# Optimization experiments

Hardware: AMD Instinct MI355X
Metric: run time of the kernel (lower is better)

The kernel has to match this reference:

```python
import jax, jax.numpy as jnp
import numpy as np

EPS = 1e-12  # torch F.normalize default eps

def _l1_normalize(x):
    # F.normalize(x, p=1, dim=1): divide by channel-wise L1 norm, clamped at eps
    n = jnp.sum(jnp.abs(x), axis=1, keepdims=True)
    return x / jnp.maximum(n, EPS)

def setup_inputs() -> dict:
    key = jax.random.key(0)
    k1, k2, k3 = jax.random.split(key, 3)
    shape = (2, 128, 64, 64)  # B, C, H, W
    return {
        "a": jax.random.normal(k1, shape, dtype=jnp.float32),
        "b": jax.random.normal(k2, shape, dtype=jnp.float32),
        "c": jax.random.normal(k3, shape, dtype=jnp.float32),
    }

def reference(a, b, c):
    a = _l1_normalize(a)
    b = _l1_normalize(b)
    c = _l1_normalize(c)
    sim_ab = jnp.einsum('bchw,bcij->bhwij', a, b)
    sim_ac = jnp.einsum('bchw,bcij->bhwij', a, c)
    # F.l1_loss default reduction='mean'
    return jnp.mean(jnp.abs(sim_ac - sim_ab))
```

## Files before the change

kernel.cpp:

```cpp
#include <hip/hip_runtime.h>
#include <stdint.h>

#define HW 4096
#define NC 128
#define BATCH 2

typedef __attribute__((ext_vector_type(8))) short bf16x8;
typedef __attribute__((ext_vector_type(4))) float f32x4;
typedef __attribute__((ext_vector_type(8))) unsigned short u16x8;

__device__ __forceinline__ unsigned short f32_to_bf16(float f) {
    union { float f; unsigned int u; } v; v.f = f;
    unsigned int u = v.u;
    unsigned int r = (u + 0x7FFFu + ((u >> 16) & 1u)) >> 16;
    return (unsigned short)r;
}

__device__ __forceinline__ void async_cp16(const void* g, void* s) {
    __builtin_amdgcn_global_load_lds(
        (const __attribute__((address_space(1))) uint32_t*)g,
        (__attribute__((address_space(3))) uint32_t*)s, 16, 0, 0);
}

__global__ __launch_bounds__(512) void norm_kernel(
    const float* __restrict__ A, const float* __restrict__ B,
    const float* __restrict__ Cc,
    unsigned short* __restrict__ anT, unsigned short* __restrict__ dT,
    float* __restrict__ out) {
    const int tid = threadIdx.x;
    if (blockIdx.x == 0 && tid == 0) *out = 0.f;
    const int pl = tid & 31;
    const int cg = tid >> 5;
    const int gp = blockIdx.x * 32;
    const int bb = gp >> 12;
    const int p  = (gp & (HW - 1)) + pl;
    const size_t base = (size_t)bb * NC * HW + p;
    const int c0 = cg * 8;

    float va[8], vb[8], vc[8];
    float sa = 0.f, sb = 0.f, sc = 0.f;
#pragma unroll
    for (int k = 0; k < 8; ++k) {
        size_t idx = base + (size_t)(c0 + k) * HW;
        va[k] = A[idx]; vb[k] = B[idx]; vc[k] = Cc[idx];
        sa += fabsf(va[k]); sb += fabsf(vb[k]); sc += fabsf(vc[k]);
    }
    __shared__ float red[3][16][32];
    red[0][cg][pl] = sa; red[1][cg][pl] = sb; red[2][cg][pl] = sc;
    __syncthreads();
    float na = 0.f, nb = 0.f, nc = 0.f;
#pragma unroll
    for (int g = 0; g < 16; ++g) {
        na += red[0][g][pl]; nb += red[1][g][pl]; nc += red[2][g][pl];
    }
    const float ra = 1.f / fmaxf(na, 1e-12f);
    const float rb = 1.f / fmaxf(nb, 1e-12f);
    const float rc = 1.f / fmaxf(nc, 1e-12f);

    const size_t obase = ((size_t)bb * HW + p) * NC;
    const int slot = cg ^ (p & 15);
    u16x8 xa, xd;
#pragma unroll
    for (int j = 0; j < 8; ++j) {
        xa[j] = f32_to_bf16(va[j] * ra);
        xd[j] = f32_to_bf16(vc[j] * rc - vb[j] * rb);
    }
    *(u16x8*)(anT + obase + slot * 8) = xa;
    *(u16x8*)(dT  + obase + slot * 8) = xd;
}

__global__ __launch_bounds__(256, 2) void simloss_kernel(
    const unsigned short* __restrict__ anT, const unsigned short* __restrict__ dT,
    float* __restrict__ out) {
    __shared__ uint4 smem4[4096];
    const int tid = threadIdx.x;
    const int b   = blockIdx.x;
    const int bz  = b >> 8;
    const int my  = (b & 255) >> 3;
    const int ng  = b & 7;
    const char* gA = (const char*)(anT + ((size_t)bz * HW + my * 128) * NC);
    const char* gB0 = (const char*)(dT + ((size_t)bz * HW + ng * 4 * 128) * NC);

    const int wv  = tid >> 6;
    const int ln  = tid & 63;
    char* sA = (char*)smem4;
    char* sB = (char*)(smem4 + 2048);

#pragma unroll
    for (int i = 0; i < 8; ++i) {
        const size_t goff = (size_t)(i * 256 + tid) * 16;
        const size_t loff = (size_t)i * 4096 + wv * 1024;
        async_cp16(gA + goff, sA + loff);
        async_cp16(gB0 + goff, sB + loff);
    }
    __syncthreads();

    const int m16  = ln & 15;
    const int quad = ln >> 4;
    const int wr   = (wv >> 1) * 64;
    const int wc   = (wv & 1) * 64;

    float s = 0.f;
    for (int j = 0; j < 4; ++j) {
        f32x4 acc[4][4] = {};
#pragma unroll
        for (int ks = 0; ks < 4; ++ks) {
            const int chunk = ks * 4 + quad;
            const int slot  = chunk ^ m16;
            bf16x8 af[4], bfr[4];
#pragma unroll
            for (int mi = 0; mi < 4; ++mi)
                af[mi] = *(const bf16x8*)(sA + (wr + mi * 16 + m16) * 256 + slot * 16);
#pragma unroll
            for (int ni = 0; ni < 4; ++ni)
                bfr[ni] = *(const bf16x8*)(sB + (wc + ni * 16 + m16) * 256 + slot * 16);
#pragma unroll
            for (int mi = 0; mi < 4; ++mi)
#pragma unroll
                for (int ni = 0; ni < 4; ++ni)
                    acc[mi][ni] = __builtin_amdgcn_mfma_f32_16x16x32_bf16(
                        af[mi], bfr[ni], acc[mi][ni], 0, 0, 0);
        }
#pragma unroll
        for (int mi = 0; mi < 4; ++mi)
#pragma unroll
            for (int ni = 0; ni < 4; ++ni)
#pragma unroll
                for (int r = 0; r < 4; ++r)
                    s += fabsf(acc[mi][ni][r]);

        __syncthreads();
        if (j < 3) {
            const char* gBn = gB0 + (size_t)(j + 1) * 32768;
#pragma unroll
            for (int i = 0; i < 8; ++i) {
                const size_t goff = (size_t)(i * 256 + tid) * 16;
                const size_t loff = (size_t)i * 4096 + wv * 1024;
                async_cp16(gBn + goff, sB + loff);
            }
            __syncthreads();
        }
    }

#pragma unroll
    for (int off = 32; off > 0; off >>= 1)
        s += __shfl_down(s, off);
    if (ln == 0) ((float*)smem4)[wv] = s;
    __syncthreads();
    if (tid == 0) {
        const float inv = 1.0f / ((float)BATCH * (float)HW * (float)HW);
        float t = ((float*)smem4)[0] + ((float*)smem4)[1] +
                  ((float*)smem4)[2] + ((float*)smem4)[3];
        atomicAdd(out, t * inv);
    }
}

extern "C" void kernel_launch(void* const* d_in, const int* in_sizes, int n_in,
                              void* d_out, int out_size, void* d_ws, size_t ws_size,
                              hipStream_t stream) {
    const float* A  = (const float*)d_in[0];
    const float* B  = (const float*)d_in[1];
    const float* Cc = (const float*)d_in[2];
    float* out = (float*)d_out;
    unsigned short* anT = (unsigned short*)d_ws;
    unsigned short* dT  = anT + (size_t)BATCH * HW * NC;

    norm_kernel<<<dim3(256), dim3(512), 0, stream>>>(A, B, Cc, anT, dT, out);
    simloss_kernel<<<dim3(512), dim3(256), 0, stream>>>(anT, dT, out);
}
```

Baseline: 79.71 us.

## Fuse normalize and similarity-loss kernels with a grid barrier; register-prefetch B tiles

Merges the normalization pass and the MFMA similarity-loss pass into one persistent launch of 512 blocks, separated by a software grid-wide barrier built on a global atomic counter. This removes a kernel launch and the gap between the two kernels. It also replaces the async global-to-LDS copies of the next B tile with register prefetches issued before the MFMA loop and written to LDS afterward, so the loads overlap compute. The risks are deadlock if all 512 blocks are not co-resident, barrier spin overhead, and higher register pressure from the prefetch buffers.

```diff
diff --git a/kernel.cpp b/kernel.cpp
--- a/kernel.cpp
+++ b/kernel.cpp
@@ -4,10 +4,13 @@
 #define HW 4096
 #define NC 128
 #define BATCH 2
+#define NBLK 512
 
 typedef __attribute__((ext_vector_type(8))) short bf16x8;
 typedef __attribute__((ext_vector_type(4))) float f32x4;
 typedef __attribute__((ext_vector_type(8))) unsigned short u16x8;
+
+__device__ unsigned int g_barrier = 0;
 
 __device__ __forceinline__ unsigned short f32_to_bf16(float f) {
     union { float f; unsigned int u; } v; v.f = f;
@@ -22,67 +25,81 @@
         (__attribute__((address_space(3))) uint32_t*)s, 16, 0, 0);
 }
 
-__global__ __launch_bounds__(512) void norm_kernel(
+__global__ __launch_bounds__(256, 2) void fused_kernel(
     const float* __restrict__ A, const float* __restrict__ B,
     const float* __restrict__ Cc,
     unsigned short* __restrict__ anT, unsigned short* __restrict__ dT,
     float* __restrict__ out) {
-    const int tid = threadIdx.x;
-    if (blockIdx.x == 0 && tid == 0) *out = 0.f;
-    const int pl = tid & 31;
-    const int cg = tid >> 5;
-    const int gp = blockIdx.x * 32;
-    const int bb = gp >> 12;
-    const int p  = (gp & (HW - 1)) + pl;
-    const size_t base = (size_t)bb * NC * HW + p;
-    const int c0 = cg * 8;
-
-    float va[8], vb[8], vc[8];
-    float sa = 0.f, sb = 0.f, sc = 0.f;
-#pragma unroll
-    for (int k = 0; k < 8; ++k) {
-        size_t idx = base + (size_t)(c0 + k) * HW;
-        va[k] = A[idx]; vb[k] = B[idx]; vc[k] = Cc[idx];
-        sa += fabsf(va[k]); sb += fabsf(vb[k]); sc += fabsf(vc[k]);
-    }
-    __shared__ float red[3][16][32];
-    red[0][cg][pl] = sa; red[1][cg][pl] = sb; red[2][cg][pl] = sc;
-    __syncthreads();
-    float na = 0.f, nb = 0.f, nc = 0.f;
-#pragma unroll
-    for (int g = 0; g < 16; ++g) {
-        na += red[0][g][pl]; nb += red[1][g][pl]; nc += red[2][g][pl];
-    }
-    const float ra = 1.f / fmaxf(na, 1e-12f);
-    const float rb = 1.f / fmaxf(nb, 1e-12f);
-    const float rc = 1.f / fmaxf(nc, 1e-12f);
-
-    const size_t obase = ((size_t)bb * HW + p) * NC;
-    const int slot = cg ^ (p & 15);
-    u16x8 xa, xd;
-#pragma unroll
-    for (int j = 0; j < 8; ++j) {
-        xa[j] = f32_to_bf16(va[j] * ra);
-        xd[j] = f32_to_bf16(vc[j] * rc - vb[j] * rb);
-    }
-    *(u16x8*)(anT + obase + slot * 8) = xa;
-    *(u16x8*)(dT  + obase + slot * 8) = xd;
-}
-
-__global__ __launch_bounds__(256, 2) void simloss_kernel(
-    const unsigned short* __restrict__ anT, const unsigned short* __restrict__ dT,
-    float* __restrict__ out) {
     __shared__ uint4 smem4[4096];
     const int tid = threadIdx.x;
     const int b   = blockIdx.x;
+
+    {
+        if (b == 0 && tid == 0) *out = 0.f;
+        const int pl = tid & 15;
+        const int cg = tid >> 4;
+        const int gp = b * 16;
+        const int bb = gp >> 12;
+        const int p  = (gp & (HW - 1)) + pl;
+        const size_t base = (size_t)bb * NC * HW + p;
+        const int c0 = cg * 8;
+
+        float va[8], vb[8], vc[8];
+        float sa = 0.f, sb = 0.f, sc = 0.f;
+#pragma unroll
+        for (int k = 0; k < 8; ++k) {
+            size_t idx = base + (size_t)(c0 + k) * HW;
+            va[k] = A[idx]; vb[k] = B[idx]; vc[k] = Cc[idx];
+            sa += fabsf(va[k]); sb += fabsf(vb[k]); sc += fabsf(vc[k]);
+        }
+        float* red = (float*)smem4;
+        red[(0 * 16 + cg) * 16 + pl] = sa;
+        red[(1 * 16 + cg) * 16 + pl] = sb;
+        red[(2 * 16 + cg) * 16 + pl] = sc;
+        __syncthreads();
+        float na = 0.f, nb = 0.f, nc = 0.f;
+#pragma unroll
+        for (int g = 0; g < 16; ++g) {
+            na += red[(0 * 16 + g) * 16 + pl];
+            nb += red[(1 * 16 + g) * 16 + pl];
+            nc += red[(2 * 16 + g) * 16 + pl];
+        }
+        const float ra = 1.f / fmaxf(na, 1e-12f);
+        const float rb = 1.f / fmaxf(nb, 1e-12f);
+        const float rc = 1.f / fmaxf(nc, 1e-12f);
+
+        const size_t obase = ((size_t)bb * HW + p) * NC;
+        const int slot = cg ^ (p & 15);
+        u16x8 xa, xd;
+#pragma unroll
+        for (int j = 0; j < 8; ++j) {
+            xa[j] = f32_to_bf16(va[j] * ra);
+            xd[j] = f32_to_bf16(vc[j] * rc - vb[j] * rb);
+        }
+        *(u16x8*)(anT + obase + slot * 8) = xa;
+        *(u16x8*)(dT  + obase + slot * 8) = xd;
+    }
+
+    __threadfence();
+    __syncthreads();
+    if (tid == 0) {
+        unsigned int old = atomicAdd(&g_barrier, 1u);
+        unsigned int target = (old & ~(unsigned)(NBLK - 1)) + NBLK;
+        while ((int)(__hip_atomic_load(&g_barrier, __ATOMIC_RELAXED,
+                                       __HIP_MEMORY_SCOPE_AGENT) - target) < 0)
+            __builtin_amdgcn_s_sleep(2);
+    }
+    __syncthreads();
+    __threadfence();
+
     const int bz  = b >> 8;
     const int my  = (b & 255) >> 3;
     const int ng  = b & 7;
-    const char* gA = (const char*)(anT + ((size_t)bz * HW + my * 128) * NC);
-    const char* gB0 = (const char*)(dT + ((size_t)bz * HW + ng * 4 * 128) * NC);
+    const char* gA  = (const char*)(anT + ((size_t)bz * HW + my * 128) * NC);
+    const char* gB0 = (const char*)(dT  + ((size_t)bz * HW + ng * 4 * 128) * NC);
 
-    const int wv  = tid >> 6;
-    const int ln  = tid & 63;
+    const int wv = tid >> 6;
+    const int ln = tid & 63;
     char* sA = (char*)smem4;
     char* sB = (char*)(smem4 + 2048);
 
@@ -101,7 +118,14 @@
     const int wc   = (wv & 1) * 64;
 
     float s = 0.f;
+    uint4 pb[8];
     for (int j = 0; j < 4; ++j) {
+        if (j < 3) {
+            const char* gBn = gB0 + (size_t)(j + 1) * 32768;
+#pragma unroll
+            for (int i = 0; i < 8; ++i)
+                pb[i] = *(const uint4*)(gBn + (size_t)(i * 256 + tid) * 16);
+        }
         f32x4 acc[4][4] = {};
 #pragma unroll
         for (int ks = 0; ks < 4; ++ks) {
@@ -131,13 +155,9 @@
 
         __syncthreads();
         if (j < 3) {
-            const char* gBn = gB0 + (size_t)(j + 1) * 32768;
 #pragma unroll
-            for (int i = 0; i < 8; ++i) {
-                const size_t goff = (size_t)(i * 256 + tid) * 16;
-                const size_t loff = (size_t)i * 4096 + wv * 1024;
-                async_cp16(gBn + goff, sB + loff);
-            }
+            for (int i = 0; i < 8; ++i)
+                *(uint4*)(sB + (size_t)i * 4096 + tid * 16) = pb[i];
             __syncthreads();
         }
     }
@@ -165,6 +185,5 @@
     unsigned short* anT = (unsigned short*)d_ws;
     unsigned short* dT  = anT + (size_t)BATCH * HW * NC;
 
-    norm_kernel<<<dim3(256), dim3(512), 0, stream>>>(A, B, Cc, anT, dT, out);
-    simloss_kernel<<<dim3(512), dim3(256), 0, stream>>>(anT, dT, out);
+    fused_kernel<<<dim3(NBLK), dim3(256), 0, stream>>>(A, B, Cc, anT, dT, out);
 }
```

Measured after the change: 190.4 us. 139% more time.
